# Kernel optimization log

Hardware: AMD Instinct MI355X
Metric: run time of the kernel (lower is better)

## Reference

```python
import jax, jax.numpy as jnp
import numpy as np

N_NODES = 100000
N_EDGES = 600000
N_GRAPHS = 512
F_IN = 128
F_HID = 128
F_OUT = 128


def setup_inputs() -> dict:
    key = jax.random.key(0)
    ks = jax.random.split(key, 10)
    x = jax.random.normal(ks[0], (N_NODES, F_IN), dtype=jnp.float32)
    edge_index = jax.random.randint(ks[1], (2, N_EDGES), 0, N_NODES, dtype=jnp.int64)
    batch = jnp.sort(jax.random.randint(ks[2], (N_NODES,), 0, N_GRAPHS, dtype=jnp.int64))
    s1 = 1.0 / np.sqrt(F_IN)
    s2 = 1.0 / np.sqrt(F_HID)
    s3 = 1.0 / np.sqrt(F_OUT)
    W1 = jax.random.uniform(ks[3], (F_IN, F_HID), jnp.float32, -s1, s1)
    b1 = jnp.zeros((F_HID,), jnp.float32)
    W2 = jax.random.uniform(ks[4], (F_HID, F_OUT), jnp.float32, -s2, s2)
    b2 = jnp.zeros((F_OUT,), jnp.float32)
    Wlin = jax.random.uniform(ks[5], (F_OUT, 1), jnp.float32, -s3, s3)
    blin = jax.random.uniform(ks[6], (1,), jnp.float32, -s3, s3)
    return {"x": x, "edge_index": edge_index, "batch": batch,
            "W1": W1, "b1": b1, "W2": W2, "b2": b2, "Wlin": Wlin, "blin": blin}


def reference(x, edge_index, batch, W1, b1, W2, b2, Wlin, blin):
    N = x.shape[0]
    # GCN normalization with self-loops: D^{-1/2} (A + I) D^{-1/2}
    loop = jnp.arange(N, dtype=edge_index.dtype)
    src = jnp.concatenate([edge_index[0], loop])  # [E + N]
    dst = jnp.concatenate([edge_index[1], loop])
    deg = jax.ops.segment_sum(jnp.ones_like(dst, dtype=x.dtype), dst, num_segments=N)
    dis = jnp.where(deg > 0, jax.lax.rsqrt(jnp.maximum(deg, 1.0)), 0.0)  # deg^{-1/2}
    norm = (dis[src] * dis[dst])[:, None]  # [E+N, 1] edge weights

    def gcn_conv(h, W, b):
        hW = h @ W                                      # [N, d_out]
        msgs = norm * hW[src]                           # gather + scale
        agg = jax.ops.segment_sum(msgs, dst, num_segments=N)  # scatter-add
        return agg + b

    h = jax.nn.relu(gcn_conv(x, W1, b1))
    h = gcn_conv(h, W2, b2)

    # global_mean_pool over graph ids
    counts = jax.ops.segment_sum(jnp.ones((N,), x.dtype), batch, num_segments=N_GRAPHS)
    pooled = jax.ops.segment_sum(h, batch, num_segments=N_GRAPHS)
    pooled = pooled / jnp.maximum(counts, 1.0)[:, None]  # [N_GRAPHS, F_OUT]

    # dropout is identity in eval mode
    return pooled @ Wlin + blin  # [N_GRAPHS, 1]
```

## Files before the change

kernel.cpp:

```cpp
#include <hip/hip_runtime.h>

#define F 128
#define CAP 64

typedef _Float16 f16x8 __attribute__((ext_vector_type(8)));
typedef float f32x4 __attribute__((ext_vector_type(4)));

__global__ __launch_bounds__(256) void k_prep(const float* __restrict__ W1, const float* __restrict__ W2,
                                              const float* __restrict__ Wlin, const float* __restrict__ b2,
                                              const float* __restrict__ blin, const int* __restrict__ batch,
                                              const int* __restrict__ src, const int* __restrict__ dst,
                                              _Float16* __restrict__ Bswz, float* __restrict__ w2l,
                                              float* __restrict__ cconst, int* __restrict__ gstart,
                                              int* __restrict__ cnt, int* __restrict__ srcs,
                                              int N, int E, int G, int bG) {
    int bid = blockIdx.x;
    int tid = threadIdx.x;
    if (bid < 64) {
        int o = bid * 256 + tid;
        int j = o & 7, lane = (o >> 3) & 63, tc = o >> 9;
        int t = tc >> 3, c = tc & 7;
        int k = t * 32 + (lane >> 4) * 8 + j;
        int n = c * 16 + (lane & 15);
        Bswz[o] = (_Float16)W1[k * F + n];
    } else if (bid == 64) {
        __shared__ float sh[F];
        if (tid < F) {
            float s = 0.0f;
            for (int j = 0; j < F; j += 4) {
                float4 w = *(const float4*)&W2[tid * F + j];
                float4 l = *(const float4*)&Wlin[j];
                s += w.x * l.x + w.y * l.y + w.z * l.z + w.w * l.w;
            }
            w2l[tid] = s;
            sh[tid] = b2[tid] * Wlin[tid];
        }
        __syncthreads();
        if (tid == 0) {
            float c = blin[0];
            for (int j = 0; j < F; ++j) c += sh[j];
            *cconst = c;
        }
    } else if (bid < 65 + bG) {
        int g = (bid - 65) * 256 + tid;
        if (g < G) {
            int lo = 0, hi = N;
            while (lo < hi) { int mid = (lo + hi) >> 1; if (batch[mid] < g) lo = mid + 1; else hi = mid; }
            gstart[g] = lo;
            if (g == 0) gstart[G] = N;
        }
    } else {
        int e = (bid - 65 - bG) * 256 + tid;
        if (e < E) {
            int s = src[e], d = dst[e];
            int slot = atomicAdd(&cnt[d], 1);
            srcs[d * CAP + slot] = s;
        }
    }
}

__global__ __launch_bounds__(256) void k_gemm_mfma(const float* __restrict__ X,
                                                   const _Float16* __restrict__ Bswz,
                                                   const int* __restrict__ cnt,
                                                   float* __restrict__ dis,
                                                   _Float16* __restrict__ Yb, int N) {
    int lane = threadIdx.x & 63, wave = threadIdx.x >> 6;
    int quad = lane >> 4, m = lane & 15;
    int r0 = blockIdx.x * 128 + wave * 32;

    f32x4 acc[2][8];
#pragma unroll
    for (int rt = 0; rt < 2; ++rt)
#pragma unroll
        for (int c = 0; c < 8; ++c) acc[rt][c] = (f32x4)0.0f;

    int ra = r0 + m;      if (ra >= N) ra = N - 1;
    int rb = r0 + 16 + m; if (rb >= N) rb = N - 1;
    const float* pxa = &X[(size_t)ra * F + quad * 8];
    const float* pxb = &X[(size_t)rb * F + quad * 8];

    float4 a0 = *(const float4*)pxa, a1 = *(const float4*)(pxa + 4);
    float4 a2 = *(const float4*)pxb, a3 = *(const float4*)(pxb + 4);

#pragma unroll 1
    for (int t = 0; t < 4; ++t) {
        const _Float16* bp = Bswz + (size_t)t * 4096 + lane * 8;
        f16x8 B[8];
#pragma unroll
        for (int c = 0; c < 8; ++c) B[c] = *(const f16x8*)(bp + c * 512);

        float fa[8] = {a0.x, a0.y, a0.z, a0.w, a1.x, a1.y, a1.z, a1.w};
        float fb[8] = {a2.x, a2.y, a2.z, a2.w, a3.x, a3.y, a3.z, a3.w};
        f16x8 A0, A1;
#pragma unroll
        for (int j = 0; j < 8; ++j) {
            A0[j] = (_Float16)fa[j];
            A1[j] = (_Float16)fb[j];
        }
        if (t < 3) {
            a0 = *(const float4*)(pxa + (t + 1) * 32);
            a1 = *(const float4*)(pxa + (t + 1) * 32 + 4);
            a2 = *(const float4*)(pxb + (t + 1) * 32);
            a3 = *(const float4*)(pxb + (t + 1) * 32 + 4);
        }
#pragma unroll
        for (int c = 0; c < 8; ++c) {
            acc[0][c] = __builtin_amdgcn_mfma_f32_16x16x32_f16(A0, B[c], acc[0][c], 0, 0, 0);
            acc[1][c] = __builtin_amdgcn_mfma_f32_16x16x32_f16(A1, B[c], acc[1][c], 0, 0, 0);
        }
    }

#pragma unroll
    for (int rt = 0; rt < 2; ++rt) {
        int rbase = r0 + rt * 16 + quad * 4;
#pragma unroll
        for (int r = 0; r < 4; ++r) {
            int row = rbase + r;
            if (row < N) {
                float dr = rsqrtf((float)cnt[row] + 1.0f);
                if (m == 0) dis[row] = dr;
#pragma unroll
                for (int c = 0; c < 8; ++c)
                    Yb[(size_t)row * F + c * 16 + m] = (_Float16)(acc[rt][c][r] * dr);
            }
        }
    }
}

__global__ __launch_bounds__(256) void k_agg_z(const _Float16* __restrict__ hWb, const float* __restrict__ dis,
                                               const int* __restrict__ cnt, const int* __restrict__ srcs,
                                               const float* __restrict__ bias, const float* __restrict__ w2l,
                                               float* __restrict__ zt, int N) {
    __shared__ int sdeg[32], snode[32], smap[32];
    int tid = threadIdx.x;
    int nb = blockIdx.x * 32;
    if (tid < 32) {
        int n = nb + tid;
        sdeg[tid]  = (n < N) ? cnt[n] : 0x40000000;
        snode[tid] = (n < N) ? n : -1;
    }
    __syncthreads();
    if (tid < 32) {
        int v = sdeg[tid];
        int rank = 0;
#pragma unroll 8
        for (int j = 0; j < 32; ++j) {
            int vj = sdeg[j];
            rank += (vj < v) || (vj == v && j < tid);
        }
        smap[rank] = snode[tid];
    }
    __syncthreads();
    int node = smap[tid >> 3];
    if (node < 0) return;
    int lane = tid & 7;
    float di = dis[node];
    float s[16];
    {
        const _Float16* pr = &hWb[(size_t)node * F + lane * 16];
        f16x8 v0 = *(const f16x8*)pr;
        f16x8 v1 = *(const f16x8*)(pr + 8);
#pragma unroll
        for (int j = 0; j < 8; ++j) { s[j] = (float)v0[j]; s[8 + j] = (float)v1[j]; }
    }
    int e0 = node * CAP, e1 = e0 + cnt[node];
    int e = e0;
    for (; e + 4 <= e1; e += 4) {
        int i0 = srcs[e], i1 = srcs[e + 1], i2 = srcs[e + 2], i3 = srcs[e + 3];
        const _Float16* p0 = &hWb[(size_t)i0 * F + lane * 16];
        const _Float16* p1 = &hWb[(size_t)i1 * F + lane * 16];
        const _Float16* p2 = &hWb[(size_t)i2 * F + lane * 16];
        const _Float16* p3 = &hWb[(size_t)i3 * F + lane * 16];
        f16x8 a0 = *(const f16x8*)p0, b0 = *(const f16x8*)(p0 + 8);
        f16x8 a1 = *(const f16x8*)p1, b1 = *(const f16x8*)(p1 + 8);
        f16x8 a2 = *(const f16x8*)p2, b2 = *(const f16x8*)(p2 + 8);
        f16x8 a3 = *(const f16x8*)p3, b3 = *(const f16x8*)(p3 + 8);
#pragma unroll
        for (int j = 0; j < 8; ++j) {
            s[j]     += (float)a0[j] + (float)a1[j] + (float)a2[j] + (float)a3[j];
            s[8 + j] += (float)b0[j] + (float)b1[j] + (float)b2[j] + (float)b3[j];
        }
    }
    for (; e < e1; ++e) {
        const _Float16* pr = &hWb[(size_t)srcs[e] * F + lane * 16];
        f16x8 v0 = *(const f16x8*)pr;
        f16x8 v1 = *(const f16x8*)(pr + 8);
#pragma unroll
        for (int j = 0; j < 8; ++j) { s[j] += (float)v0[j]; s[8 + j] += (float)v1[j]; }
    }
    float p = 0.0f;
#pragma unroll
    for (int q = 0; q < 4; ++q) {
        float4 bb = *(const float4*)&bias[lane * 16 + q * 4];
        float4 ww = *(const float4*)&w2l[lane * 16 + q * 4];
        p += fmaxf(fmaf(di, s[q * 4 + 0], bb.x), 0.0f) * ww.x;
        p += fmaxf(fmaf(di, s[q * 4 + 1], bb.y), 0.0f) * ww.y;
        p += fmaxf(fmaf(di, s[q * 4 + 2], bb.z), 0.0f) * ww.z;
        p += fmaxf(fmaf(di, s[q * 4 + 3], bb.w), 0.0f) * ww.w;
    }
#pragma unroll
    for (int d = 1; d < 8; d <<= 1) p += __shfl_xor(p, d);
    if (lane == 0) zt[node] = di * p;
}

__global__ __launch_bounds__(256) void k_pool(const float* __restrict__ zt, const float* __restrict__ dis,
                                              const int* __restrict__ cnt, const int* __restrict__ srcs,
                                              const int* __restrict__ gstart, const float* __restrict__ cconst,
                                              const float* __restrict__ blin, float* __restrict__ out, int G) {
    int g = blockIdx.x;
    int g0 = gstart[g], g1 = gstart[g + 1];
    float acc = 0.0f;
    for (int n = g0 + threadIdx.x; n < g1; n += 256) {
        float s = zt[n];
        int e0 = n * CAP, e1 = e0 + cnt[n];
        int e = e0;
        for (; e + 4 <= e1; e += 4) {
            s += zt[srcs[e]] + zt[srcs[e + 1]] + zt[srcs[e + 2]] + zt[srcs[e + 3]];
        }
        for (; e < e1; ++e) s += zt[srcs[e]];
        acc += dis[n] * s;
    }
#pragma unroll
    for (int d = 1; d < 64; d <<= 1) acc += __shfl_xor(acc, d);
    __shared__ float ws4[4];
    if ((threadIdx.x & 63) == 0) ws4[threadIdx.x >> 6] = acc;
    __syncthreads();
    if (threadIdx.x == 0) {
        float sum = ws4[0] + ws4[1] + ws4[2] + ws4[3];
        int c = g1 - g0;
        out[g] = (c > 0) ? (sum / (float)c + cconst[0]) : blin[0];
    }
}


extern "C" void kernel_launch(void* const* d_in, const int* in_sizes, int n_in,
                              void* d_out, int out_size, void* d_ws, size_t ws_size,
                              hipStream_t stream) {
    const float* x    = (const float*)d_in[0];
    const int*   ei   = (const int*)d_in[1];
    const int*   batch= (const int*)d_in[2];
    const float* W1   = (const float*)d_in[3];
    const float* b1   = (const float*)d_in[4];
    const float* W2   = (const float*)d_in[5];
    const float* b2   = (const float*)d_in[6];
    const float* Wlin = (const float*)d_in[7];
    const float* blin = (const float*)d_in[8];
    float* out = (float*)d_out;

    const int N = in_sizes[2];
    const int E = in_sizes[1] / 2;
    const int G = out_size;
    const int* src = ei;
    const int* dst = ei + E;

    char* p = (char*)d_ws;
    auto take = [&](size_t bytes) { char* q = p; p += (bytes + 255) & ~(size_t)255; return q; };
    _Float16* hWb  = (_Float16*)take((size_t)N * F * 2);
    float*  ztbuf  = (float*)take((size_t)N * 4);
    int*    cnt    = (int*)  take((size_t)N * 4);
    float*  dis    = (float*)take((size_t)N * 4);
    int*    srcs   = (int*)  take((size_t)N * CAP * 4);
    int*    gstart = (int*)  take((size_t)(G + 1) * 4);
    float*  w2l    = (float*)take((size_t)F * 4);
    float*  cconst = (float*)take(256);
    _Float16* Bswz = (_Float16*)take((size_t)F * F * 2);

    const int nbE = (E + 255) / 256;
    const int bG  = (G + 255) / 256;

    hipMemsetAsync(cnt, 0, (size_t)N * 4, stream);

    k_prep <<<65 + bG + nbE, 256, 0, stream>>>(W1, W2, Wlin, b2, blin, batch, src, dst,
                                               Bswz, w2l, cconst, gstart, cnt, srcs, N, E, G, bG);
    k_gemm_mfma<<<(N + 127) / 128, 256, 0, stream>>>(x, Bswz, cnt, dis, hWb, N);
    k_agg_z<<<(N + 31) / 32, 256, 0, stream>>>(hWb, dis, cnt, srcs, b1, w2l, ztbuf, N);
    k_pool <<<G, 256, 0, stream>>>(ztbuf, dis, cnt, srcs, gstart, cconst, blin, out, G);
}
```

Before: 187.3 us.

## Fuse edge bucketing into GEMM kernel and compute degree norms on the fly

The memset of the degree counters moves into the prep kernel. The edge-bucketing atomics now run interleaved with the MFMA GEMM blocks in one launch (three edge blocks per GEMM block) so the scatter and the GEMM overlap. Because the GEMM can no longer wait for final degrees, source-side normalization moves into the aggregation loop: each neighbor's degree is read and rsqrt'd per edge, and the dis array is removed. This trades a launch and a memset for extra random cnt loads and FMAs in the aggregation loop.

```diff
diff --git a/kernel.cpp b/kernel.cpp
--- a/kernel.cpp
+++ b/kernel.cpp
@@ -6,14 +6,12 @@
 typedef _Float16 f16x8 __attribute__((ext_vector_type(8)));
 typedef float f32x4 __attribute__((ext_vector_type(4)));
 
-__global__ __launch_bounds__(256) void k_prep(const float* __restrict__ W1, const float* __restrict__ W2,
-                                              const float* __restrict__ Wlin, const float* __restrict__ b2,
-                                              const float* __restrict__ blin, const int* __restrict__ batch,
-                                              const int* __restrict__ src, const int* __restrict__ dst,
-                                              _Float16* __restrict__ Bswz, float* __restrict__ w2l,
-                                              float* __restrict__ cconst, int* __restrict__ gstart,
-                                              int* __restrict__ cnt, int* __restrict__ srcs,
-                                              int N, int E, int G, int bG) {
+__global__ __launch_bounds__(256) void k_prep0(const float* __restrict__ W1, const float* __restrict__ W2,
+                                               const float* __restrict__ Wlin, const float* __restrict__ b2,
+                                               const float* __restrict__ blin, const int* __restrict__ batch,
+                                               _Float16* __restrict__ Bswz, float* __restrict__ w2l,
+                                               float* __restrict__ cconst, int* __restrict__ gstart,
+                                               int* __restrict__ cnt, int N, int G, int bG) {
     int bid = blockIdx.x;
     int tid = threadIdx.x;
     if (bid < 64) {
@@ -50,23 +48,37 @@
             if (g == 0) gstart[G] = N;
         }
     } else {
-        int e = (bid - 65 - bG) * 256 + tid;
+        int idx4 = (bid - 65 - bG) * 256 + tid;
+        int i = idx4 * 4;
+        if (i + 3 < N) {
+            *(int4*)&cnt[i] = make_int4(0, 0, 0, 0);
+        } else {
+            for (int j = i; j < N; ++j) if (j >= 0) cnt[j] = 0;
+        }
+    }
+}
+
+__global__ __launch_bounds__(256) void k_fused(const float* __restrict__ X,
+                                               const _Float16* __restrict__ Bswz,
+                                               const int* __restrict__ src, const int* __restrict__ dst,
+                                               int* __restrict__ cnt, int* __restrict__ srcs,
+                                               _Float16* __restrict__ Yb, int N, int E, int nbGemm) {
+    int bid = blockIdx.x, tid = threadIdx.x;
+    int g = bid >> 2, r = bid & 3;
+    if (r != 0 || g >= nbGemm) {
+        if (r == 0) return;
+        int e = (3 * g + (r - 1)) * 256 + tid;
         if (e < E) {
             int s = src[e], d = dst[e];
             int slot = atomicAdd(&cnt[d], 1);
             srcs[d * CAP + slot] = s;
         }
-    }
-}
-
-__global__ __launch_bounds__(256) void k_gemm_mfma(const float* __restrict__ X,
-                                                   const _Float16* __restrict__ Bswz,
-                                                   const int* __restrict__ cnt,
-                                                   float* __restrict__ dis,
-                                                   _Float16* __restrict__ Yb, int N) {
-    int lane = threadIdx.x & 63, wave = threadIdx.x >> 6;
+        return;
+    }
+
+    int lane = tid & 63, wave = tid >> 6;
     int quad = lane >> 4, m = lane & 15;
-    int r0 = blockIdx.x * 128 + wave * 32;
+    int r0 = g * 128 + wave * 32;
 
     f32x4 acc[2][8];
 #pragma unroll
@@ -114,24 +126,22 @@
     for (int rt = 0; rt < 2; ++rt) {
         int rbase = r0 + rt * 16 + quad * 4;
 #pragma unroll
-        for (int r = 0; r < 4; ++r) {
-            int row = rbase + r;
+        for (int rr = 0; rr < 4; ++rr) {
+            int row = rbase + rr;
             if (row < N) {
-                float dr = rsqrtf((float)cnt[row] + 1.0f);
-                if (m == 0) dis[row] = dr;
 #pragma unroll
                 for (int c = 0; c < 8; ++c)
-                    Yb[(size_t)row * F + c * 16 + m] = (_Float16)(acc[rt][c][r] * dr);
+                    Yb[(size_t)row * F + c * 16 + m] = (_Float16)acc[rt][c][rr];
             }
         }
     }
 }
 
-__global__ __launch_bounds__(256) void k_agg_z(const _Float16* __restrict__ hWb, const float* __restrict__ dis,
+__global__ __launch_bounds__(256) void k_agg_z(const _Float16* __restrict__ hWb,
                                                const int* __restrict__ cnt, const int* __restrict__ srcs,
                                                const float* __restrict__ bias, const float* __restrict__ w2l,
                                                float* __restrict__ zt, int N) {
-    __shared__ int sdeg[32], snode[32], smap[32];
+    __shared__ int sdeg[32], snode[32], smapN[32], smapD[32];
     int tid = threadIdx.x;
     int nb = blockIdx.x * 32;
     if (tid < 32) {
@@ -148,25 +158,31 @@
             int vj = sdeg[j];
             rank += (vj < v) || (vj == v && j < tid);
         }
-        smap[rank] = snode[tid];
+        smapN[rank] = snode[tid];
+        smapD[rank] = sdeg[tid];
     }
     __syncthreads();
-    int node = smap[tid >> 3];
+    int node = smapN[tid >> 3];
     if (node < 0) return;
+    int dg = smapD[tid >> 3];
+    float di = rsqrtf((float)dg + 1.0f);
     int lane = tid & 7;
-    float di = dis[node];
     float s[16];
     {
         const _Float16* pr = &hWb[(size_t)node * F + lane * 16];
         f16x8 v0 = *(const f16x8*)pr;
         f16x8 v1 = *(const f16x8*)(pr + 8);
 #pragma unroll
-        for (int j = 0; j < 8; ++j) { s[j] = (float)v0[j]; s[8 + j] = (float)v1[j]; }
-    }
-    int e0 = node * CAP, e1 = e0 + cnt[node];
+        for (int j = 0; j < 8; ++j) { s[j] = di * (float)v0[j]; s[8 + j] = di * (float)v1[j]; }
+    }
+    int e0 = node * CAP, e1 = e0 + dg;
     int e = e0;
     for (; e + 4 <= e1; e += 4) {
         int i0 = srcs[e], i1 = srcs[e + 1], i2 = srcs[e + 2], i3 = srcs[e + 3];
+        float w0 = rsqrtf((float)cnt[i0] + 1.0f);
+        float w1 = rsqrtf((float)cnt[i1] + 1.0f);
+        float w2 = rsqrtf((float)cnt[i2] + 1.0f);
+        float w3 = rsqrtf((float)cnt[i3] + 1.0f);
         const _Float16* p0 = &hWb[(size_t)i0 * F + lane * 16];
         const _Float16* p1 = &hWb[(size_t)i1 * F + lane * 16];
         const _Float16* p2 = &hWb[(size_t)i2 * F + lane * 16];
@@ -177,16 +193,27 @@
         f16x8 a3 = *(const f16x8*)p3, b3 = *(const f16x8*)(p3 + 8);
 #pragma unroll
         for (int j = 0; j < 8; ++j) {
-            s[j]     += (float)a0[j] + (float)a1[j] + (float)a2[j] + (float)a3[j];
-            s[8 + j] += (float)b0[j] + (float)b1[j] + (float)b2[j] + (float)b3[j];
+            s[j]     = fmaf(w0, (float)a0[j], s[j]);
+            s[j]     = fmaf(w1, (float)a1[j], s[j]);
+            s[j]     = fmaf(w2, (float)a2[j], s[j]);
+            s[j]     = fmaf(w3, (float)a3[j], s[j]);
+            s[8 + j] = fmaf(w0, (float)b0[j], s[8 + j]);
+            s[8 + j] = fmaf(w1, (float)b1[j], s[8 + j]);
+            s[8 + j] = fmaf(w2, (float)b2[j], s[8 + j]);
+            s[8 + j] = fmaf(w3, (float)b3[j], s[8 + j]);
         }
     }
     for (; e < e1; ++e) {
-        const _Float16* pr = &hWb[(size_t)srcs[e] * F + lane * 16];
+        int i0 = srcs[e];
+        float w0 = rsqrtf((float)cnt[i0] + 1.0f);
+        const _Float16* pr = &hWb[(size_t)i0 * F + lane * 16];
         f16x8 v0 = *(const f16x8*)pr;
         f16x8 v1 = *(const f16x8*)(pr + 8);
 #pragma unroll
-        for (int j = 0; j < 8; ++j) { s[j] += (float)v0[j]; s[8 + j] += (float)v1[j]; }
+        for (int j = 0; j < 8; ++j) {
+            s[j]     = fmaf(w0, (float)v0[j], s[j]);
+            s[8 + j] = fmaf(w0, (float)v1[j], s[8 + j]);
+        }
     }
     float p = 0.0f;
 #pragma unroll
@@ -203,7 +230,7 @@
     if (lane == 0) zt[node] = di * p;
 }
 
-__global__ __launch_bounds__(256) void k_pool(const float* __restrict__ zt, const float* __restrict__ dis,
+__global__ __launch_bounds__(256) void k_pool(const float* __restrict__ zt,
                                               const int* __restrict__ cnt, const int* __restrict__ srcs,
                                               const int* __restrict__ gstart, const float* __restrict__ cconst,
                                               const float* __restrict__ blin, float* __restrict__ out, int G) {
@@ -212,13 +239,14 @@
     float acc = 0.0f;
     for (int n = g0 + threadIdx.x; n < g1; n += 256) {
         float s = zt[n];
-        int e0 = n * CAP, e1 = e0 + cnt[n];
+        int dg = cnt[n];
+        int e0 = n * CAP, e1 = e0 + dg;
         int e = e0;
         for (; e + 4 <= e1; e += 4) {
             s += zt[srcs[e]] + zt[srcs[e + 1]] + zt[srcs[e + 2]] + zt[srcs[e + 3]];
         }
         for (; e < e1; ++e) s += zt[srcs[e]];
-        acc += dis[n] * s;
+        acc += rsqrtf((float)dg + 1.0f) * s;
     }
 #pragma unroll
     for (int d = 1; d < 64; d <<= 1) acc += __shfl_xor(acc, d);
@@ -258,21 +286,22 @@
     _Float16* hWb  = (_Float16*)take((size_t)N * F * 2);
     float*  ztbuf  = (float*)take((size_t)N * 4);
     int*    cnt    = (int*)  take((size_t)N * 4);
-    float*  dis    = (float*)take((size_t)N * 4);
     int*    srcs   = (int*)  take((size_t)N * CAP * 4);
     int*    gstart = (int*)  take((size_t)(G + 1) * 4);
     float*  w2l    = (float*)take((size_t)F * 4);
     float*  cconst = (float*)take(256);
     _Float16* Bswz = (_Float16*)take((size_t)F * F * 2);
 
+    const int bG  = (G + 255) / 256;
+    const int zb  = (N + 1023) / 1024;
+    const int nbGemm = (N + 127) / 128;
     const int nbE = (E + 255) / 256;
-    const int bG  = (G + 255) / 256;
-
-    hipMemsetAsync(cnt, 0, (size_t)N * 4, stream);
-
-    k_prep <<<65 + bG + nbE, 256, 0, stream>>>(W1, W2, Wlin, b2, blin, batch, src, dst,
-                                               Bswz, w2l, cconst, gstart, cnt, srcs, N, E, G, bG);
-    k_gemm_mfma<<<(N + 127) / 128, 256, 0, stream>>>(x, Bswz, cnt, dis, hWb, N);
-    k_agg_z<<<(N + 31) / 32, 256, 0, stream>>>(hWb, dis, cnt, srcs, b1, w2l, ztbuf, N);
-    k_pool <<<G, 256, 0, stream>>>(ztbuf, dis, cnt, srcs, gstart, cconst, blin, out, G);
-}
+    int nbQ = nbGemm;
+    if (3 * nbQ < nbE) nbQ = (nbE + 2) / 3;
+
+    k_prep0<<<65 + bG + zb, 256, 0, stream>>>(W1, W2, Wlin, b2, blin, batch,
+                                              Bswz, w2l, cconst, gstart, cnt, N, G, bG);
+    k_fused<<<4 * nbQ, 256, 0, stream>>>(x, Bswz, src, dst, cnt, srcs, hWb, N, E, nbGemm);
+    k_agg_z<<<(N + 31) / 32, 256, 0, stream>>>(hWb, cnt, srcs, b1, w2l, ztbuf, N);
+    k_pool <<<G, 256, 0, stream>>>(ztbuf, cnt, srcs, gstart, cconst, blin, out, G);
+}
```

Measured after the change: 211.7 us. 13.1% more time.
